# Performance work log

Hardware: AMD Instinct MI355X
Metric: run time of the kernel (lower is better)

The kernel has to match this reference:

```python
import jax, jax.numpy as jnp
import numpy as np

BN_EPS = 1e-5


def setup_inputs() -> dict:
    key = jax.random.key(0)
    ks = jax.random.split(key, 6)
    B, N, M, C1, C2 = 8, 8192, 2048, 128, 256
    in_ch = C1 + C2  # 384
    return {
        "xyz1": jax.random.uniform(ks[0], (B, N, 3), dtype=jnp.float32),
        "xyz2": jax.random.uniform(ks[1], (B, M, 3), dtype=jnp.float32),
        "features1": jax.random.normal(ks[2], (B, C1, N), dtype=jnp.float32),
        "features2": jax.random.normal(ks[3], (B, C2, M), dtype=jnp.float32),
        # Conv1d(kernel_size=1, bias=False) weights, squeezed to [out, in]
        "conv_w0": jax.random.normal(ks[4], (256, in_ch), dtype=jnp.float32) * 0.05,
        "gamma0": jnp.ones((256,), dtype=jnp.float32),
        "beta0": jnp.zeros((256,), dtype=jnp.float32),
        "conv_w1": jax.random.normal(ks[5], (256, 256), dtype=jnp.float32) * 0.05,
        "gamma1": jnp.ones((256,), dtype=jnp.float32),
        "beta1": jnp.zeros((256,), dtype=jnp.float32),
    }


def _conv_bn_relu(x, w, gamma, beta):
    # 1x1 Conv1d (no bias) == per-point channel matmul: [B,Cin,N] -> [B,Cout,N]
    x = jnp.einsum("oc,bcn->bon", w, x)
    # BatchNorm1d in training mode: batch stats over (B, N), biased variance
    mu = jnp.mean(x, axis=(0, 2), keepdims=True)
    var = jnp.var(x, axis=(0, 2), keepdims=True)
    x = (x - mu) * jax.lax.rsqrt(var + BN_EPS)
    x = x * gamma[None, :, None] + beta[None, :, None]
    return jax.nn.relu(x)


def reference(xyz1, xyz2, features1, features2,
              conv_w0, gamma0, beta0, conv_w1, gamma1, beta1):
    # squared pairwise distances [B, N, M] (broadcast diff reduced over coord dim)
    diff = xyz1[:, :, None, :] - xyz2[:, None, :, :]  # [B,N,M,3]
    dists = jnp.sum(diff * diff, axis=-1)             # [B,N,M]
    idx = jnp.argmin(dists, axis=-1)                  # [B,N] nearest downsampled point

    # per-batch gather: features2[b, :, idx[b]] -> [B, C2, N]
    interp = jax.vmap(lambda f, i: f[:, i])(features2, idx)

    x = jnp.concatenate([features1, interp], axis=1)  # [B, C1+C2, N]
    x = _conv_bn_relu(x, conv_w0, gamma0, beta0)
    x = _conv_bn_relu(x, conv_w1, gamma1, beta1)
    return x
```

## Files before the change

### kernel.cpp

```cpp
#include <hip/hip_runtime.h>
#include <stdint.h>

typedef unsigned short u16;
typedef unsigned int u32;
typedef __attribute__((ext_vector_type(8))) short short8;
typedef __attribute__((ext_vector_type(4))) float floatx4;

__device__ __forceinline__ u16 f2b(float f) {
  union { float f; u32 u; } c; c.f = f;
  u32 u = c.u;
  u += 0x7fffu + ((u >> 16) & 1u);
  return (u16)(u >> 16);
}
__device__ __forceinline__ float b2f(u16 h) {
  union { u32 u; float f; } c; c.u = ((u32)h) << 16;
  return c.f;
}

__device__ __forceinline__ void glds16(const void* g, void* l) {
  __builtin_amdgcn_global_load_lds((__attribute__((address_space(1))) void*)g,
                                   (__attribute__((address_space(3))) void*)l, 16, 0, 0);
}

__global__ void cast_bf16_k(const float* __restrict__ in, u16* __restrict__ out, int n) {
  int i = blockIdx.x * 256 + threadIdx.x;
  if (i < n) out[i] = f2b(in[i]);
}

__global__ void transpose_cast_k(const float* __restrict__ in, u16* __restrict__ out, int C, int N) {
  __shared__ u16 tile[64][72];
  int b = blockIdx.z;
  int c0 = blockIdx.y * 64, n0 = blockIdx.x * 64;
  const float* src = in + ((size_t)b * C + c0) * N + n0;
  int t = threadIdx.x;
#pragma unroll
  for (int i = 0; i < 4; i++) {
    int id = t + i * 256;
    int c = id >> 4, nq = (id & 15) * 4;
    float4 v = *(const float4*)(src + (size_t)c * N + nq);
    tile[nq + 0][c] = f2b(v.x);
    tile[nq + 1][c] = f2b(v.y);
    tile[nq + 2][c] = f2b(v.z);
    tile[nq + 3][c] = f2b(v.w);
  }
  __syncthreads();
  int n = t >> 2, ch = (t & 3) * 16;
  u16* dst = out + ((size_t)b * N + n0 + n) * C + c0 + ch;
  uint4 a = *(const uint4*)&tile[n][ch];
  uint4 bb = *(const uint4*)&tile[n][ch + 8];
  *(uint4*)dst = a;
  *(uint4*)(dst + 8) = bb;
}

__global__ void argmin_part_k(const float* __restrict__ xyz1, const float* __restrict__ xyz2,
                              float2* __restrict__ cand) {
  __shared__ float4 s2[256];
  int b = blockIdx.z, mq = blockIdx.y, nq = blockIdx.x;
  const float* x2 = xyz2 + ((size_t)b * 2048 + mq * 256) * 3;
  int t = threadIdx.x;
  s2[t] = make_float4(x2[t * 3], x2[t * 3 + 1], x2[t * 3 + 2], 0.f);
  __syncthreads();
  int n0 = nq * 1024 + t;
  float px[4], py[4], pz[4];
#pragma unroll
  for (int q = 0; q < 4; q++) {
    const float* p1 = xyz1 + ((size_t)b * 8192 + n0 + q * 256) * 3;
    px[q] = p1[0]; py[q] = p1[1]; pz[q] = p1[2];
  }
  float best[4] = {3.0e38f, 3.0e38f, 3.0e38f, 3.0e38f};
  int bi[4] = {0, 0, 0, 0};
#pragma unroll 4
  for (int m = 0; m < 256; m++) {
    float4 qq = s2[m];
#pragma unroll
    for (int q = 0; q < 4; q++) {
      float dx = px[q] - qq.x, dy = py[q] - qq.y, dz = pz[q] - qq.z;
      float d = fmaf(dz, dz, fmaf(dy, dy, dx * dx));
      bool c = d < best[q];
      best[q] = c ? d : best[q];
      bi[q] = c ? m : bi[q];
    }
  }
#pragma unroll
  for (int q = 0; q < 4; q++) {
    int n = n0 + q * 256;
    cand[(size_t)mq * 65536 + (size_t)b * 8192 + n] =
        make_float2(best[q], __int_as_float(mq * 256 + bi[q]));
  }
}

__global__ void argmin_combine_k(const float2* __restrict__ cand, int* __restrict__ idx) {
  int p = blockIdx.x * 256 + threadIdx.x;
  float bd = 3.0e38f; int bi = 0;
#pragma unroll
  for (int q = 0; q < 8; q++) {
    float2 c = cand[(size_t)q * 65536 + p];
    if (c.x < bd) { bd = c.x; bi = __float_as_int(c.y); }
  }
  idx[p] = bi;
}

__global__ __launch_bounds__(256) void gemm1_k(const u16* __restrict__ w0b, const u16* __restrict__ f1t,
                                               const u16* __restrict__ f2t, const int* __restrict__ idx,
                                               u16* __restrict__ y0) {
  __shared__ u16 As[128 * 64];
  __shared__ u16 Bs[128 * 64];
  __shared__ int sidx[128];
  int t = threadIdx.x;
  int pt0 = blockIdx.x * 128, o0 = blockIdx.y * 128;
  int b = pt0 >> 13;
  if (t < 128) sidx[t] = idx[pt0 + t];
  floatx4 zero = {0.f, 0.f, 0.f, 0.f};
  floatx4 acc[4][4];
#pragma unroll
  for (int i = 0; i < 4; i++)
#pragma unroll
    for (int j = 0; j < 4; j++) acc[i][j] = zero;
  int lane = t & 63, wave = t >> 6;
  int wrow = (wave >> 1) * 64, wcol = (wave & 1) * 64;
  int lr = lane & 15, lq = lane >> 4;
  int srow = lane >> 3;
  int sch = ((lane & 7) ^ srow) * 8;
  __syncthreads();
  int rowS[4], gidxB[4];
#pragma unroll
  for (int i = 0; i < 4; i++) {
    rowS[i] = (i * 4 + wave) * 8 + srow;
    gidxB[i] = sidx[rowS[i]];
  }

#pragma unroll
  for (int k0 = 0; k0 < 384; k0 += 64) {
    __syncthreads();
#pragma unroll
    for (int i = 0; i < 4; i++)
      glds16(w0b + (size_t)(o0 + rowS[i]) * 384 + k0 + sch, &As[(i * 4 + wave) * 512]);
    if (k0 < 128) {
#pragma unroll
      for (int i = 0; i < 4; i++)
        glds16(f1t + (size_t)(pt0 + rowS[i]) * 128 + k0 + sch, &Bs[(i * 4 + wave) * 512]);
    } else {
#pragma unroll
      for (int i = 0; i < 4; i++)
        glds16(f2t + ((size_t)(b << 11) + gidxB[i]) * 256 + (k0 - 128) + sch, &Bs[(i * 4 + wave) * 512]);
    }
    __syncthreads();
#pragma unroll
    for (int ks = 0; ks < 2; ks++) {
      short8 af[4], bf[4];
#pragma unroll
      for (int i = 0; i < 4; i++) {
        int row = wrow + i * 16 + lr;
        af[i] = *(const short8*)&As[row * 64 + ((((ks << 2) | lq) ^ (lr & 7)) << 3)];
      }
#pragma unroll
      for (int j = 0; j < 4; j++) {
        int row = wcol + j * 16 + lr;
        bf[j] = *(const short8*)&Bs[row * 64 + ((((ks << 2) | lq) ^ (lr & 7)) << 3)];
      }
#pragma unroll
      for (int i = 0; i < 4; i++)
#pragma unroll
        for (int j = 0; j < 4; j++)
          acc[i][j] = __builtin_amdgcn_mfma_f32_16x16x32_bf16(af[i], bf[j], acc[i][j], 0, 0, 0);
    }
  }
#pragma unroll
  for (int i = 0; i < 4; i++) {
#pragma unroll
    for (int j = 0; j < 4; j++) {
      int o = o0 + wrow + i * 16 + lq * 4;
      int p = pt0 + wcol + j * 16 + lr;
      uint2 pk;
      pk.x = (u32)f2b(acc[i][j][0]) | ((u32)f2b(acc[i][j][1]) << 16);
      pk.y = (u32)f2b(acc[i][j][2]) | ((u32)f2b(acc[i][j][3]) << 16);
      *(uint2*)&y0[(size_t)p * 256 + o] = pk;
    }
  }
}

__global__ __launch_bounds__(256) void gemm2_k(const u16* __restrict__ w1b, const u16* __restrict__ y0,
                                               const float* __restrict__ scale0, const float* __restrict__ shift0,
                                               u16* __restrict__ y1) {
  __shared__ u16 As[128 * 64];
  __shared__ u16 Bs[128 * 72];
  __shared__ float ssc[256], ssh[256];
  int t = threadIdx.x;
  ssc[t] = scale0[t];
  ssh[t] = shift0[t];
  int pt0 = blockIdx.x * 128, o0 = blockIdx.y * 128;
  floatx4 zero = {0.f, 0.f, 0.f, 0.f};
  floatx4 acc[4][4];
#pragma unroll
  for (int i = 0; i < 4; i++)
#pragma unroll
    for (int j = 0; j < 4; j++) acc[i][j] = zero;
  int lane = t & 63, wave = t >> 6;
  int wrow = (wave >> 1) * 64, wcol = (wave & 1) * 64;
  int lr = lane & 15, lq = lane >> 4;
  int srow = lane >> 3;
  int sch = ((lane & 7) ^ srow) * 8;
  __syncthreads();

#pragma unroll
  for (int k0 = 0; k0 < 256; k0 += 64) {
    __syncthreads();
#pragma unroll
    for (int i = 0; i < 4; i++) {
      int rowA = (i * 4 + wave) * 8 + srow;
      glds16(w1b + (size_t)(o0 + rowA) * 256 + k0 + sch, &As[(i * 4 + wave) * 512]);
    }
#pragma unroll
    for (int i = 0; i < 4; i++) {
      int id = t + i * 256;
      int row = id >> 3, ch = (id & 7) * 8;
      uint4 raw = *(const uint4*)(y0 + (size_t)(pt0 + row) * 256 + k0 + ch);
      u32 rw[4] = {raw.x, raw.y, raw.z, raw.w};
      u32 ow[4];
#pragma unroll
      for (int w = 0; w < 4; w++) {
        int k = k0 + ch + w * 2;
        float v0 = b2f((u16)(rw[w] & 0xffffu));
        float v1 = b2f((u16)(rw[w] >> 16));
        v0 = fmaxf(v0 * ssc[k] + ssh[k], 0.f);
        v1 = fmaxf(v1 * ssc[k + 1] + ssh[k + 1], 0.f);
        ow[w] = (u32)f2b(v0) | ((u32)f2b(v1) << 16);
      }
      uint4 ov; ov.x = ow[0]; ov.y = ow[1]; ov.z = ow[2]; ov.w = ow[3];
      *(uint4*)&Bs[row * 72 + ch] = ov;
    }
    __syncthreads();
#pragma unroll
    for (int ks = 0; ks < 2; ks++) {
      int kk = ks * 32 + lq * 8;
      short8 af[4], bf[4];
#pragma unroll
      for (int i = 0; i < 4; i++) {
        int row = wrow + i * 16 + lr;
        af[i] = *(const short8*)&As[row * 64 + ((((ks << 2) | lq) ^ (lr & 7)) << 3)];
      }
#pragma unroll
      for (int j = 0; j < 4; j++) bf[j] = *(const short8*)&Bs[(wcol + j * 16 + lr) * 72 + kk];
#pragma unroll
      for (int i = 0; i < 4; i++)
#pragma unroll
        for (int j = 0; j < 4; j++)
          acc[i][j] = __builtin_amdgcn_mfma_f32_16x16x32_bf16(af[i], bf[j], acc[i][j], 0, 0, 0);
    }
  }
#pragma unroll
  for (int i = 0; i < 4; i++) {
#pragma unroll
    for (int j = 0; j < 4; j++) {
      int o = o0 + wrow + i * 16 + lq * 4;
      int p = pt0 + wcol + j * 16 + lr;
      uint2 pk;
      pk.x = (u32)f2b(acc[i][j][0]) | ((u32)f2b(acc[i][j][1]) << 16);
      pk.y = (u32)f2b(acc[i][j][2]) | ((u32)f2b(acc[i][j][3]) << 16);
      *(uint2*)&y1[(size_t)p * 256 + o] = pk;
    }
  }
}

__global__ void stats_k(const u16* __restrict__ y, float* __restrict__ sum, float* __restrict__ sq) {
  int o = threadIdx.x;
  const u16* base = y + (size_t)blockIdx.x * 65536 + o;
  float s = 0.f, q = 0.f;
  for (int p = 0; p < 256; p++) {
    float v = b2f(base[(size_t)p * 256]);
    s += v; q += v * v;
  }
  atomicAdd(&sum[o], s);
  atomicAdd(&sq[o], q);
}

__global__ void bnparam_k(const float* __restrict__ sum, const float* __restrict__ sq,
                          const float* __restrict__ gamma, const float* __restrict__ beta,
                          float* __restrict__ scale, float* __restrict__ shift) {
  int o = threadIdx.x;
  float mean = sum[o] * (1.f / 65536.f);
  float var = sq[o] * (1.f / 65536.f) - mean * mean;
  var = fmaxf(var, 0.f);
  float r = rsqrtf(var + 1e-5f);
  float sc = gamma[o] * r;
  scale[o] = sc;
  shift[o] = beta[o] - mean * sc;
}

__global__ void finalize_k(const u16* __restrict__ y1, const float* __restrict__ scale,
                           const float* __restrict__ shift, float* __restrict__ out) {
  __shared__ float tile[64][65];
  int b = blockIdx.z, o0 = blockIdx.y * 64, n0 = blockIdx.x * 64;
  int t = threadIdx.x;
  int pl = t >> 2, ch = (t & 3) * 16;
  const u16* src = y1 + ((size_t)(b * 8192 + n0 + pl)) * 256 + o0 + ch;
  uint4 r0 = *(const uint4*)src;
  uint4 r1 = *(const uint4*)(src + 8);
  u16 hv[16];
  *(uint4*)&hv[0] = r0;
  *(uint4*)&hv[8] = r1;
#pragma unroll
  for (int e = 0; e < 16; e++) {
    int o = o0 + ch + e;
    float v = b2f(hv[e]) * scale[o] + shift[o];
    tile[pl][ch + e] = fmaxf(v, 0.f);
  }
  __syncthreads();
  int ol = t >> 2, nch = (t & 3) * 16;
  float* dst = out + ((size_t)(b * 256 + o0 + ol)) * 8192 + n0 + nch;
#pragma unroll
  for (int j = 0; j < 16; j += 4) {
    float4 v = make_float4(tile[nch + j][ol], tile[nch + j + 1][ol],
                           tile[nch + j + 2][ol], tile[nch + j + 3][ol]);
    *(float4*)(dst + j) = v;
  }
}

extern "C" void kernel_launch(void* const* d_in, const int* in_sizes, int n_in,
                              void* d_out, int out_size, void* d_ws, size_t ws_size,
                              hipStream_t stream) {
  const float* xyz1      = (const float*)d_in[0];
  const float* xyz2      = (const float*)d_in[1];
  const float* features1 = (const float*)d_in[2];
  const float* features2 = (const float*)d_in[3];
  const float* conv_w0   = (const float*)d_in[4];
  const float* gamma0    = (const float*)d_in[5];
  const float* beta0     = (const float*)d_in[6];
  const float* conv_w1   = (const float*)d_in[7];
  const float* gamma1    = (const float*)d_in[8];
  const float* beta1     = (const float*)d_in[9];
  float* out = (float*)d_out;

  char* ws = (char*)d_ws;
  size_t off = 0;
  auto alloc = [&](size_t bytes) {
    char* p = ws + off;
    off = (off + bytes + 4095) & ~(size_t)4095;
    return p;
  };
  int*   idx    = (int*)alloc(65536 * 4);
  float* sums   = (float*)alloc(4 * 256 * 4);
  float* params = (float*)alloc(4 * 256 * 4);
  u16*   w0b    = (u16*)alloc(256 * 384 * 2);
  u16*   w1b    = (u16*)alloc(256 * 256 * 2);
  u16*   f1t    = (u16*)alloc((size_t)65536 * 128 * 2);
  u16*   f2t    = (u16*)alloc((size_t)16384 * 256 * 2);
  u16*   y0     = (u16*)alloc((size_t)65536 * 256 * 2);
  u16*   y1     = (u16*)alloc((size_t)65536 * 256 * 2);
  float2* cand  = (float2*)f1t;

  hipMemsetAsync(sums, 0, 4 * 256 * 4, stream);
  cast_bf16_k<<<dim3(384), 256, 0, stream>>>(conv_w0, w0b, 98304);
  cast_bf16_k<<<dim3(256), 256, 0, stream>>>(conv_w1, w1b, 65536);
  argmin_part_k<<<dim3(8, 8, 8), 256, 0, stream>>>(xyz1, xyz2, cand);
  argmin_combine_k<<<dim3(256), 256, 0, stream>>>(cand, idx);
  transpose_cast_k<<<dim3(128, 2, 8), 256, 0, stream>>>(features1, f1t, 128, 8192);
  transpose_cast_k<<<dim3(32, 4, 8), 256, 0, stream>>>(features2, f2t, 256, 2048);
  gemm1_k<<<dim3(512, 2), 256, 0, stream>>>(w0b, f1t, f2t, idx, y0);
  stats_k<<<dim3(256), 256, 0, stream>>>(y0, sums + 0, sums + 256);
  bnparam_k<<<1, 256, 0, stream>>>(sums + 0, sums + 256, gamma0, beta0, params + 0, params + 256);
  gemm2_k<<<dim3(512, 2), 256, 0, stream>>>(w1b, y0, params + 0, params + 256, y1);
  stats_k<<<dim3(256), 256, 0, stream>>>(y1, sums + 512, sums + 768);
  bnparam_k<<<1, 256, 0, stream>>>(sums + 512, sums + 768, gamma1, beta1, params + 512, params + 768);
  finalize_k<<<dim3(128, 4, 8), 256, 0, stream>>>(y1, params + 512, params + 768, out);
}
```

Measured before the change: 268.7 us.

## Fuse small kernels, widen GEMM blocks to full output width, vectorize stats

Several small steps are folded into their neighbours. The weight casts and the sums memset merge into one prep kernel, the argmin combine moves into the gemm1 prologue, and the BN parameter computation moves into the gemm2 and finalize prologues. Both GEMMs now use 512-thread blocks that cover all 256 output channels, so the activation tile is loaded and gathered once instead of twice. stats_k is rewritten to do coalesced 16-byte loads with a shared-memory reduction. This cuts launch count and redundant B-tile traffic, at the cost of larger LDS per block and BN parameters being recomputed in every block.

After: 249.9 us. -7.0%, faster.

```diff
diff --git a/kernel.cpp b/kernel.cpp
--- a/kernel.cpp
+++ b/kernel.cpp
@@ -22,9 +22,13 @@
                                    (__attribute__((address_space(3))) void*)l, 16, 0, 0);
 }
 
-__global__ void cast_bf16_k(const float* __restrict__ in, u16* __restrict__ out, int n) {
-  int i = blockIdx.x * 256 + threadIdx.x;
-  if (i < n) out[i] = f2b(in[i]);
+__global__ void prep_k(const float* __restrict__ w0, const float* __restrict__ w1,
+                       u16* __restrict__ w0b, u16* __restrict__ w1b, float* __restrict__ sums) {
+  int blk = blockIdx.x, t = threadIdx.x;
+  int i = blk * 256 + t;
+  if (blk < 384) w0b[i] = f2b(w0[i]);
+  else { int j = i - 98304; w1b[j] = f2b(w1[j]); }
+  if (blk < 4) sums[i] = 0.f;
 }
 
 __global__ void transpose_cast_k(const float* __restrict__ in, u16* __restrict__ out, int C, int N) {
@@ -89,27 +93,25 @@
   }
 }
 
-__global__ void argmin_combine_k(const float2* __restrict__ cand, int* __restrict__ idx) {
-  int p = blockIdx.x * 256 + threadIdx.x;
-  float bd = 3.0e38f; int bi = 0;
-#pragma unroll
-  for (int q = 0; q < 8; q++) {
-    float2 c = cand[(size_t)q * 65536 + p];
-    if (c.x < bd) { bd = c.x; bi = __float_as_int(c.y); }
-  }
-  idx[p] = bi;
-}
-
-__global__ __launch_bounds__(256) void gemm1_k(const u16* __restrict__ w0b, const u16* __restrict__ f1t,
-                                               const u16* __restrict__ f2t, const int* __restrict__ idx,
+__global__ __launch_bounds__(512) void gemm1_k(const u16* __restrict__ w0b, const u16* __restrict__ f1t,
+                                               const u16* __restrict__ f2t, const float2* __restrict__ cand,
                                                u16* __restrict__ y0) {
-  __shared__ u16 As[128 * 64];
+  __shared__ u16 As[256 * 64];
   __shared__ u16 Bs[128 * 64];
   __shared__ int sidx[128];
   int t = threadIdx.x;
-  int pt0 = blockIdx.x * 128, o0 = blockIdx.y * 128;
+  int pt0 = blockIdx.x * 128;
   int b = pt0 >> 13;
-  if (t < 128) sidx[t] = idx[pt0 + t];
+  if (t < 128) {
+    int p = pt0 + t;
+    float bd = 3.0e38f; int bi = 0;
+#pragma unroll
+    for (int qc = 0; qc < 8; qc++) {
+      float2 c = cand[(size_t)qc * 65536 + p];
+      if (c.x < bd) { bd = c.x; bi = __float_as_int(c.y); }
+    }
+    sidx[t] = bi;
+  }
   floatx4 zero = {0.f, 0.f, 0.f, 0.f};
   floatx4 acc[4][4];
 #pragma unroll
@@ -122,27 +124,29 @@
   int srow = lane >> 3;
   int sch = ((lane & 7) ^ srow) * 8;
   __syncthreads();
-  int rowS[4], gidxB[4];
-#pragma unroll
-  for (int i = 0; i < 4; i++) {
-    rowS[i] = (i * 4 + wave) * 8 + srow;
-    gidxB[i] = sidx[rowS[i]];
+  int prow[2], gidx[2];
+#pragma unroll
+  for (int i = 0; i < 2; i++) {
+    prow[i] = (wave * 2 + i) * 8 + srow;
+    gidx[i] = sidx[prow[i]];
   }
 
 #pragma unroll
   for (int k0 = 0; k0 < 384; k0 += 64) {
     __syncthreads();
 #pragma unroll
-    for (int i = 0; i < 4; i++)
-      glds16(w0b + (size_t)(o0 + rowS[i]) * 384 + k0 + sch, &As[(i * 4 + wave) * 512]);
+    for (int i = 0; i < 4; i++) {
+      int chunkA = wave * 4 + i;
+      glds16(w0b + (size_t)(chunkA * 8 + srow) * 384 + k0 + sch, &As[chunkA * 512]);
+    }
     if (k0 < 128) {
 #pragma unroll
-      for (int i = 0; i < 4; i++)
-        glds16(f1t + (size_t)(pt0 + rowS[i]) * 128 + k0 + sch, &Bs[(i * 4 + wave) * 512]);
+      for (int i = 0; i < 2; i++)
+        glds16(f1t + (size_t)(pt0 + prow[i]) * 128 + k0 + sch, &Bs[(wave * 2 + i) * 512]);
     } else {
 #pragma unroll
-      for (int i = 0; i < 4; i++)
-        glds16(f2t + ((size_t)(b << 11) + gidxB[i]) * 256 + (k0 - 128) + sch, &Bs[(i * 4 + wave) * 512]);
+      for (int i = 0; i < 2; i++)
+        glds16(f2t + ((size_t)(b << 11) + gidx[i]) * 256 + (k0 - 128) + sch, &Bs[(wave * 2 + i) * 512]);
     }
     __syncthreads();
 #pragma unroll
@@ -169,7 +173,7 @@
   for (int i = 0; i < 4; i++) {
 #pragma unroll
     for (int j = 0; j < 4; j++) {
-      int o = o0 + wrow + i * 16 + lq * 4;
+      int o = wrow + i * 16 + lq * 4;
       int p = pt0 + wcol + j * 16 + lr;
       uint2 pk;
       pk.x = (u32)f2b(acc[i][j][0]) | ((u32)f2b(acc[i][j][1]) << 16);
@@ -179,16 +183,23 @@
   }
 }
 
-__global__ __launch_bounds__(256) void gemm2_k(const u16* __restrict__ w1b, const u16* __restrict__ y0,
-                                               const float* __restrict__ scale0, const float* __restrict__ shift0,
+__global__ __launch_bounds__(512) void gemm2_k(const u16* __restrict__ w1b, const u16* __restrict__ y0,
+                                               const float* __restrict__ sum0, const float* __restrict__ sq0,
+                                               const float* __restrict__ gamma0, const float* __restrict__ beta0,
                                                u16* __restrict__ y1) {
-  __shared__ u16 As[128 * 64];
+  __shared__ u16 As[256 * 64];
   __shared__ u16 Bs[128 * 72];
   __shared__ float ssc[256], ssh[256];
   int t = threadIdx.x;
-  ssc[t] = scale0[t];
-  ssh[t] = shift0[t];
-  int pt0 = blockIdx.x * 128, o0 = blockIdx.y * 128;
+  if (t < 256) {
+    float mean = sum0[t] * (1.f / 65536.f);
+    float var = fmaxf(sq0[t] * (1.f / 65536.f) - mean * mean, 0.f);
+    float r = rsqrtf(var + 1e-5f);
+    float sc = gamma0[t] * r;
+    ssc[t] = sc;
+    ssh[t] = beta0[t] - mean * sc;
+  }
+  int pt0 = blockIdx.x * 128;
   floatx4 zero = {0.f, 0.f, 0.f, 0.f};
   floatx4 acc[4][4];
 #pragma unroll
@@ -200,19 +211,18 @@
   int lr = lane & 15, lq = lane >> 4;
   int srow = lane >> 3;
   int sch = ((lane & 7) ^ srow) * 8;
-  __syncthreads();
 
 #pragma unroll
   for (int k0 = 0; k0 < 256; k0 += 64) {
     __syncthreads();
 #pragma unroll
     for (int i = 0; i < 4; i++) {
-      int rowA = (i * 4 + wave) * 8 + srow;
-      glds16(w1b + (size_t)(o0 + rowA) * 256 + k0 + sch, &As[(i * 4 + wave) * 512]);
-    }
-#pragma unroll
-    for (int i = 0; i < 4; i++) {
-      int id = t + i * 256;
+      int chunkA = wave * 4 + i;
+      glds16(w1b + (size_t)(chunkA * 8 + srow) * 256 + k0 + sch, &As[chunkA * 512]);
+    }
+#pragma unroll
+    for (int i = 0; i < 2; i++) {
+      int id = t + i * 512;
       int row = id >> 3, ch = (id & 7) * 8;
       uint4 raw = *(const uint4*)(y0 + (size_t)(pt0 + row) * 256 + k0 + ch);
       u32 rw[4] = {raw.x, raw.y, raw.z, raw.w};
@@ -252,7 +262,7 @@
   for (int i = 0; i < 4; i++) {
 #pragma unroll
     for (int j = 0; j < 4; j++) {
-      int o = o0 + wrow + i * 16 + lq * 4;
+      int o = wrow + i * 16 + lq * 4;
       int p = pt0 + wcol + j * 16 + lr;
       uint2 pk;
       pk.x = (u32)f2b(acc[i][j][0]) | ((u32)f2b(acc[i][j][1]) << 16);
@@ -263,35 +273,55 @@
 }
 
 __global__ void stats_k(const u16* __restrict__ y, float* __restrict__ sum, float* __restrict__ sq) {
-  int o = threadIdx.x;
-  const u16* base = y + (size_t)blockIdx.x * 65536 + o;
-  float s = 0.f, q = 0.f;
-  for (int p = 0; p < 256; p++) {
-    float v = b2f(base[(size_t)p * 256]);
-    s += v; q += v * v;
-  }
-  atomicAdd(&sum[o], s);
-  atomicAdd(&sq[o], q);
-}
-
-__global__ void bnparam_k(const float* __restrict__ sum, const float* __restrict__ sq,
-                          const float* __restrict__ gamma, const float* __restrict__ beta,
-                          float* __restrict__ scale, float* __restrict__ shift) {
-  int o = threadIdx.x;
-  float mean = sum[o] * (1.f / 65536.f);
-  float var = sq[o] * (1.f / 65536.f) - mean * mean;
-  var = fmaxf(var, 0.f);
-  float r = rsqrtf(var + 1e-5f);
-  float sc = gamma[o] * r;
-  scale[o] = sc;
-  shift[o] = beta[o] - mean * sc;
-}
-
-__global__ void finalize_k(const u16* __restrict__ y1, const float* __restrict__ scale,
-                           const float* __restrict__ shift, float* __restrict__ out) {
+  __shared__ float ls[8][256];
+  __shared__ float lqd[8][256];
+  int t = threadIdx.x;
+  int c8 = (t & 31) * 8;
+  int p0 = t >> 5;
+  float s[8] = {0.f, 0.f, 0.f, 0.f, 0.f, 0.f, 0.f, 0.f};
+  float q[8] = {0.f, 0.f, 0.f, 0.f, 0.f, 0.f, 0.f, 0.f};
+  const u16* base = y + (size_t)blockIdx.x * 65536;
+  for (int it = 0; it < 32; it++) {
+    int p = p0 + it * 8;
+    uint4 raw = *(const uint4*)(base + (size_t)p * 256 + c8);
+    u32 rw[4] = {raw.x, raw.y, raw.z, raw.w};
+#pragma unroll
+    for (int w = 0; w < 4; w++) {
+      float v0 = b2f((u16)(rw[w] & 0xffffu));
+      float v1 = b2f((u16)(rw[w] >> 16));
+      s[w * 2] += v0;     q[w * 2] += v0 * v0;
+      s[w * 2 + 1] += v1; q[w * 2 + 1] += v1 * v1;
+    }
+  }
+#pragma unroll
+  for (int e = 0; e < 8; e++) { ls[p0][c8 + e] = s[e]; lqd[p0][c8 + e] = q[e]; }
+  __syncthreads();
+  if (t < 256) {
+    float ss = 0.f, qq = 0.f;
+#pragma unroll
+    for (int r = 0; r < 8; r++) { ss += ls[r][t]; qq += lqd[r][t]; }
+    atomicAdd(&sum[t], ss);
+    atomicAdd(&sq[t], qq);
+  }
+}
+
+__global__ void finalize_k(const u16* __restrict__ y1, const float* __restrict__ sum1,
+                           const float* __restrict__ sq1, const float* __restrict__ gamma1,
+                           const float* __restrict__ beta1, float* __restrict__ out) {
   __shared__ float tile[64][65];
+  __shared__ float fs[64], fh[64];
   int b = blockIdx.z, o0 = blockIdx.y * 64, n0 = blockIdx.x * 64;
   int t = threadIdx.x;
+  if (t < 64) {
+    int o = o0 + t;
+    float mean = sum1[o] * (1.f / 65536.f);
+    float var = fmaxf(sq1[o] * (1.f / 65536.f) - mean * mean, 0.f);
+    float r = rsqrtf(var + 1e-5f);
+    float sc = gamma1[o] * r;
+    fs[t] = sc;
+    fh[t] = beta1[o] - mean * sc;
+  }
+  __syncthreads();
   int pl = t >> 2, ch = (t & 3) * 16;
   const u16* src = y1 + ((size_t)(b * 8192 + n0 + pl)) * 256 + o0 + ch;
   uint4 r0 = *(const uint4*)src;
@@ -301,8 +331,7 @@
   *(uint4*)&hv[8] = r1;
 #pragma unroll
   for (int e = 0; e < 16; e++) {
-    int o = o0 + ch + e;
-    float v = b2f(hv[e]) * scale[o] + shift[o];
+    float v = b2f(hv[e]) * fs[ch + e] + fh[ch + e];
     tile[pl][ch + e] = fmaxf(v, 0.f);
   }
   __syncthreads();
@@ -338,29 +367,22 @@
     off = (off + bytes + 4095) & ~(size_t)4095;
     return p;
   };
-  int*   idx    = (int*)alloc(65536 * 4);
-  float* sums   = (float*)alloc(4 * 256 * 4);
-  float* params = (float*)alloc(4 * 256 * 4);
-  u16*   w0b    = (u16*)alloc(256 * 384 * 2);
-  u16*   w1b    = (u16*)alloc(256 * 256 * 2);
-  u16*   f1t    = (u16*)alloc((size_t)65536 * 128 * 2);
-  u16*   f2t    = (u16*)alloc((size_t)16384 * 256 * 2);
-  u16*   y0     = (u16*)alloc((size_t)65536 * 256 * 2);
-  u16*   y1     = (u16*)alloc((size_t)65536 * 256 * 2);
-  float2* cand  = (float2*)f1t;
-
-  hipMemsetAsync(sums, 0, 4 * 256 * 4, stream);
-  cast_bf16_k<<<dim3(384), 256, 0, stream>>>(conv_w0, w0b, 98304);
-  cast_bf16_k<<<dim3(256), 256, 0, stream>>>(conv_w1, w1b, 65536);
+  float*  sums = (float*)alloc(4 * 256 * 4);
+  u16*    w0b  = (u16*)alloc(256 * 384 * 2);
+  u16*    w1b  = (u16*)alloc(256 * 256 * 2);
+  float2* cand = (float2*)alloc((size_t)8 * 65536 * 8);
+  u16*    f1t  = (u16*)alloc((size_t)65536 * 128 * 2);
+  u16*    f2t  = (u16*)alloc((size_t)16384 * 256 * 2);
+  u16*    y0   = (u16*)alloc((size_t)65536 * 256 * 2);
+  u16*    y1   = (u16*)alloc((size_t)65536 * 256 * 2);
+
+  prep_k<<<dim3(640), 256, 0, stream>>>(conv_w0, conv_w1, w0b, w1b, sums);
   argmin_part_k<<<dim3(8, 8, 8), 256, 0, stream>>>(xyz1, xyz2, cand);
-  argmin_combine_k<<<dim3(256), 256, 0, stream>>>(cand, idx);
   transpose_cast_k<<<dim3(128, 2, 8), 256, 0, stream>>>(features1, f1t, 128, 8192);
   transpose_cast_k<<<dim3(32, 4, 8), 256, 0, stream>>>(features2, f2t, 256, 2048);
-  gemm1_k<<<dim3(512, 2), 256, 0, stream>>>(w0b, f1t, f2t, idx, y0);
+  gemm1_k<<<dim3(512), 512, 0, stream>>>(w0b, f1t, f2t, cand, y0);
   stats_k<<<dim3(256), 256, 0, stream>>>(y0, sums + 0, sums + 256);
-  bnparam_k<<<1, 256, 0, stream>>>(sums + 0, sums + 256, gamma0, beta0, params + 0, params + 256);
-  gemm2_k<<<dim3(512, 2), 256, 0, stream>>>(w1b, y0, params + 0, params + 256, y1);
+  gemm2_k<<<dim3(512), 512, 0, stream>>>(w1b, y0, sums + 0, sums + 256, gamma0, beta0, y1);
   stats_k<<<dim3(256), 256, 0, stream>>>(y1, sums + 512, sums + 768);
-  bnparam_k<<<1, 256, 0, stream>>>(sums + 512, sums + 768, gamma1, beta1, params + 512, params + 768);
-  finalize_k<<<dim3(128, 4, 8), 256, 0, stream>>>(y1, params + 512, params + 768, out);
-}
+  finalize_k<<<dim3(128, 4, 8), 256, 0, stream>>>(y1, sums + 512, sums + 768, gamma1, beta1, out);
+}
```
